# Performance work log

Measured on AMD Instinct MI355X. Metric: run time of the kernel, lower is better.

Reference implementation:

```python
import jax, jax.numpy as jnp
import numpy as np

D_MODEL, D_K, D_V = 1024, 64, 64
B, S = 2, 4096
NEG = 1e9


def setup_inputs() -> dict:
    key = jax.random.key(0)
    ks = jax.random.split(key, 10)
    Q = jax.random.normal(ks[0], (B, S, D_MODEL), dtype=jnp.float32)
    K = jax.random.normal(ks[1], (B, S, D_MODEL), dtype=jnp.float32)
    V = jax.random.normal(ks[2], (B, S, D_MODEL), dtype=jnp.float32)
    mask = jax.random.randint(ks[3], (B, S, S), 0, 2, dtype=jnp.int32)
    sc = 1.0 / np.sqrt(D_MODEL)
    Wq = jax.random.normal(ks[4], (D_K, D_MODEL), dtype=jnp.float32) * sc
    bq = jnp.zeros((D_K,), dtype=jnp.float32)
    Wk = jax.random.normal(ks[5], (D_K, D_MODEL), dtype=jnp.float32) * sc
    bk = jnp.zeros((D_K,), dtype=jnp.float32)
    Wv = jax.random.normal(ks[6], (D_V, D_MODEL), dtype=jnp.float32) * sc
    bv = jnp.zeros((D_V,), dtype=jnp.float32)
    return {"Q": Q, "K": K, "V": V, "mask": mask,
            "Wq": Wq, "bq": bq, "Wk": Wk, "bk": bk, "Wv": Wv, "bv": bv}


def reference(Q, K, V, mask, Wq, bq, Wk, bk, Wv, bv):
    # Linear projections: q,k -> [B,S,d_k], v -> [B,S,d_v]
    q = jnp.einsum('bsm,km->bsk', Q, Wq) + bq
    k = jnp.einsum('bsm,km->bsk', K, Wk) + bk
    v = jnp.einsum('bsm,vm->bsv', V, Wv) + bv
    # Scaled dot-product scores [B,S,S]
    x = jnp.einsum('bqk,bsk->bqs', q, k) / jnp.sqrt(jnp.float32(D_K))
    m = mask.astype(x.dtype)
    x = x * m - NEG * (1.0 - m)
    x = jax.nn.softmax(x, axis=2)
    y = jnp.einsum('bqs,bsv->bqv', x, v)
    return y
```

## Files before the change

### kernel.cpp

```cpp
#include <hip/hip_runtime.h>

typedef unsigned short u16;
typedef unsigned long long u64;
typedef __bf16 bf16x8 __attribute__((ext_vector_type(8)));
typedef float f32x4 __attribute__((ext_vector_type(4)));
typedef int i32x4 __attribute__((ext_vector_type(4)));

#define MFMA16(a, b, c) __builtin_amdgcn_mfma_f32_16x16x32_bf16((a), (b), (c), 0, 0, 0)

__device__ __forceinline__ bf16x8 ld8(const u16* p) {
    return *reinterpret_cast<const bf16x8*>(p);
}

__device__ __forceinline__ unsigned pk2(float a, float b) {
    unsigned short ua = __builtin_bit_cast(unsigned short, (__bf16)a);
    unsigned short ub = __builtin_bit_cast(unsigned short, (__bf16)b);
    return (unsigned)ua | ((unsigned)ub << 16);
}

__device__ __forceinline__ bf16x8 cvt8(f32x4 a, f32x4 b) {
    bf16x8 r;
    r[0] = (__bf16)a[0]; r[1] = (__bf16)a[1]; r[2] = (__bf16)a[2]; r[3] = (__bf16)a[3];
    r[4] = (__bf16)b[0]; r[5] = (__bf16)b[1]; r[6] = (__bf16)b[2]; r[7] = (__bf16)b[3];
    return r;
}

__device__ __forceinline__ f32x4 ntf4(const float* p) {
    return __builtin_nontemporal_load(reinterpret_cast<const f32x4*>(p));
}
__device__ __forceinline__ i32x4 nti4(const int* p) {
    return __builtin_nontemporal_load(reinterpret_cast<const i32x4*>(p));
}

__global__ __launch_bounds__(256) void wcvt_kernel(
    const float* __restrict__ Wq, const float* __restrict__ Wk,
    const float* __restrict__ Wv, u16* __restrict__ wb)
{
    const int t = blockIdx.x * 256 + threadIdx.x;
    const int mat = t >> 13;
    const int idx = (t & 8191) * 8;
    const float* src = (mat == 0) ? Wq : (mat == 1) ? Wk : Wv;
    const f32x4 a = *(const f32x4*)(src + idx);
    const f32x4 b = *(const f32x4*)(src + idx + 4);
    uint4 o;
    o.x = pk2(a[0], a[1]); o.y = pk2(a[2], a[3]);
    o.z = pk2(b[0], b[1]); o.w = pk2(b[2], b[3]);
    *reinterpret_cast<uint4*>(wb + (size_t)mat * 65536 + idx) = o;
}

__global__ __launch_bounds__(256) void fused_kernel(
    const float* __restrict__ Q, const float* __restrict__ K, const float* __restrict__ V,
    const float* __restrict__ bq, const float* __restrict__ bk, const float* __restrict__ bv,
    const u16* __restrict__ wb, const int* __restrict__ mask,
    u16* __restrict__ qb, u16* __restrict__ kb, u16* __restrict__ vtb,
    u64* __restrict__ bits)
{
    const int lane = threadIdx.x & 63, w = threadIdx.x >> 6;

    if (blockIdx.x >= 384) {
        const int row = (blockIdx.x - 384) * 4 + w;
        const int* mp = mask + (size_t)row * 4096 + lane * 4;
        u64* op = bits + (size_t)row * 64;

        i32x4 h0[8], h1[8];
        #pragma unroll
        for (int j = 0; j < 8; ++j) h0[j] = nti4(mp + j * 256);
        #pragma unroll
        for (int j = 0; j < 8; ++j) h1[j] = nti4(mp + 2048 + j * 256);

        u64 mine0 = 0, mine1 = 0;
        #pragma unroll
        for (int j = 0; j < 8; ++j) {
            const u64 b0 = __ballot(h0[j][0] != 0);
            const u64 b1 = __ballot(h0[j][1] != 0);
            const u64 b2 = __ballot(h0[j][2] != 0);
            const u64 b3 = __ballot(h0[j][3] != 0);
            if (lane == j * 4 + 0) mine0 = b0;
            if (lane == j * 4 + 1) mine0 = b1;
            if (lane == j * 4 + 2) mine0 = b2;
            if (lane == j * 4 + 3) mine0 = b3;
            const u64 c0 = __ballot(h1[j][0] != 0);
            const u64 c1 = __ballot(h1[j][1] != 0);
            const u64 c2 = __ballot(h1[j][2] != 0);
            const u64 c3 = __ballot(h1[j][3] != 0);
            if (lane == j * 4 + 0) mine1 = c0;
            if (lane == j * 4 + 1) mine1 = c1;
            if (lane == j * 4 + 2) mine1 = c2;
            if (lane == j * 4 + 3) mine1 = c3;
        }
        if (lane < 32) { op[lane] = mine0; op[32 + lane] = mine1; }
        return;
    }

    const int mat  = blockIdx.x >> 7;
    const int tile = blockIdx.x & 127;
    const int c = lane & 15, g = lane >> 4;

    const float* X = (mat == 0) ? Q : (mat == 1) ? K : V;
    const u16*   W = wb + (size_t)mat * 65536;

    const int rw = tile * 64 + w * 16;
    const float* xp = X + (size_t)(rw + c) * 1024 + g * 8;
    const u16*   wp = W + (size_t)c * 1024 + g * 8;

    f32x4 acc[4] = {};

    f32x4 A[4], B[4];
    #pragma unroll
    for (int j = 0; j < 4; ++j) {
        A[j] = ntf4(xp + j * 32);
        B[j] = ntf4(xp + j * 32 + 4);
    }

    #pragma unroll
    for (int kk = 0; kk < 32; ++kk) {
        const bf16x8 a = cvt8(A[kk & 3], B[kk & 3]);
        if (kk < 28) {
            A[kk & 3] = ntf4(xp + (kk + 4) * 32);
            B[kk & 3] = ntf4(xp + (kk + 4) * 32 + 4);
        }
        const u16* wk = wp + kk * 32;
        if (mat < 2) {
            #pragma unroll
            for (int t = 0; t < 4; ++t)
                acc[t] = MFMA16(a, ld8(wk + t * 16384), acc[t]);
        } else {
            #pragma unroll
            for (int t = 0; t < 4; ++t)
                acc[t] = MFMA16(ld8(wk + t * 16384), a, acc[t]);
        }
    }

    if (mat < 2) {
        const float* bias = (mat == 0) ? bq : bk;
        u16* dst = (mat == 0) ? qb : kb;
        #pragma unroll
        for (int t = 0; t < 4; ++t) {
            const float bz = bias[t * 16 + c];
            #pragma unroll
            for (int r = 0; r < 4; ++r) {
                const int row = rw + g * 4 + r;
                dst[(size_t)row * 64 + t * 16 + c] =
                    __builtin_bit_cast(u16, (__bf16)(acc[t][r] + bz));
            }
        }
    } else {
        const int sg = rw + c;
        const int bidx = sg >> 12, sin = sg & 4095;
        #pragma unroll
        for (int t = 0; t < 4; ++t) {
            #pragma unroll
            for (int r = 0; r < 4; ++r) {
                const int dv = t * 16 + g * 4 + r;
                vtb[(size_t)(bidx * 64 + dv) * 4096 + sin] =
                    __builtin_bit_cast(u16, (__bf16)(acc[t][r] + bv[dv]));
            }
        }
    }
}

__global__ __launch_bounds__(256) void attn_kernel(
    const u64* __restrict__ bits, const u16* __restrict__ qb,
    const u16* __restrict__ kb, const u16* __restrict__ vtb,
    float* __restrict__ pacc, float* __restrict__ pm, float* __restrict__ pl)
{
    __shared__ uint2 plds[4][128];
    const int lane = threadIdx.x & 63, w = threadIdx.x >> 6;
    const int c = lane & 15, g = lane >> 4;
    const int gw    = blockIdx.x * 4 + w;
    const int strip = gw >> 3;
    const int chunk = gw & 7;
    const int b     = strip >> 8;
    const int q0    = (strip & 255) * 16;
    const int sBase = chunk * 512;
    const float SSC = 0.18033688011112042f;

    const u16* qrow = qb + (size_t)((b << 12) + q0 + c) * 64 + g * 8;
    const bf16x8 qf0 = ld8(qrow);
    const bf16x8 qf1 = ld8(qrow + 32);

    const u16* kfp = kb  + (((size_t)b << 12) + sBase + c) * 64 + g * 8;
    const u16* vfp = vtb + (size_t)(b * 64 + c) * 4096 + sBase + g * 8;

    const u64* bp = bits + (size_t)((b << 12) + q0 + c) * 64 + chunk * 8;
    const u64 Wd0 = bp[0], Wd1 = bp[1], Wd2 = bp[2], Wd3 = bp[3];
    const u64 Wd4 = bp[4], Wd5 = bp[5], Wd6 = bp[6], Wd7 = bp[7];

    f32x4 acc0 = {}, acc1 = {}, acc2 = {}, acc3 = {};
    const f32x4 zf = {};
    float m_run = -__builtin_inff(), l_run = 0.f;

    bf16x8 k00 = ld8(kfp),            k01 = ld8(kfp + 32);
    bf16x8 k10 = ld8(kfp + 16 * 64),  k11 = ld8(kfp + 16 * 64 + 32);

    #pragma unroll
    for (int half = 0; half < 2; ++half) {
        const u64 Wr0 = half ? Wd4 : Wd0;
        const u64 Wr1 = half ? Wd5 : Wd1;
        const u64 Wr2 = half ? Wd6 : Wd2;
        const u64 Wr3 = half ? Wd7 : Wd3;
        #pragma unroll 1
        for (int it2 = 0; it2 < 8; ++it2) {
            const int it = half * 8 + it2;

            const u16* vp = vfp + it * 32;
            const bf16x8 v0 = ld8(vp);
            const bf16x8 v1 = ld8(vp + 16 * 4096);
            const bf16x8 v2 = ld8(vp + 32 * 4096);
            const bf16x8 v3 = ld8(vp + 48 * 4096);

            f32x4 d0 = MFMA16(k00, qf0, zf);
            d0 = MFMA16(k01, qf1, d0);
            f32x4 d1 = MFMA16(k10, qf0, zf);
            d1 = MFMA16(k11, qf1, d1);

            const int no = (it < 15) ? (it + 1) * 2048 : it * 2048;
            k00 = ld8(kfp + no);            k01 = ld8(kfp + no + 32);
            k10 = ld8(kfp + no + 16 * 64);  k11 = ld8(kfp + no + 16 * 64 + 32);

            const int sh = it2 * 8 + g;
            const unsigned t0 = (unsigned)(Wr0 >> sh);
            const unsigned t1 = (unsigned)(Wr1 >> sh);
            const unsigned t2 = (unsigned)(Wr2 >> sh);
            const unsigned t3 = (unsigned)(Wr3 >> sh);

            const float x0 = (t0 & 1u)  ? d0[0] * SSC : -1e9f;
            const float x1 = (t1 & 1u)  ? d0[1] * SSC : -1e9f;
            const float x2 = (t2 & 1u)  ? d0[2] * SSC : -1e9f;
            const float x3 = (t3 & 1u)  ? d0[3] * SSC : -1e9f;
            const float x4 = (t0 & 16u) ? d1[0] * SSC : -1e9f;
            const float x5 = (t1 & 16u) ? d1[1] * SSC : -1e9f;
            const float x6 = (t2 & 16u) ? d1[2] * SSC : -1e9f;
            const float x7 = (t3 & 16u) ? d1[3] * SSC : -1e9f;

            float tm = fmaxf(fmaxf(fmaxf(x0, x1), fmaxf(x2, x3)),
                             fmaxf(fmaxf(x4, x5), fmaxf(x6, x7)));
            tm = fmaxf(tm, __shfl_xor(tm, 16));
            tm = fmaxf(tm, __shfl_xor(tm, 32));
            const float m_new = fmaxf(m_run, tm);
            const float f = exp2f(m_run - m_new);

            const float p0 = exp2f(x0 - m_new), p1 = exp2f(x1 - m_new);
            const float p2 = exp2f(x2 - m_new), p3 = exp2f(x3 - m_new);
            const float p4 = exp2f(x4 - m_new), p5 = exp2f(x5 - m_new);
            const float p6 = exp2f(x6 - m_new), p7 = exp2f(x7 - m_new);
            float rs = ((p0 + p1) + (p2 + p3)) + ((p4 + p5) + (p6 + p7));
            rs += __shfl_xor(rs, 16);
            rs += __shfl_xor(rs, 32);
            l_run = l_run * f + rs;
            m_run = m_new;

            plds[w][c * 8 + ( g      ^ (c & 7))] = make_uint2(pk2(p0, p1), pk2(p2, p3));
            plds[w][c * 8 + ((g + 4) ^ (c & 7))] = make_uint2(pk2(p4, p5), pk2(p6, p7));

            if (__any(f < 1.0f)) {
                const float f0 = __shfl(f, g * 4 + 0);
                const float f1 = __shfl(f, g * 4 + 1);
                const float f2 = __shfl(f, g * 4 + 2);
                const float f3 = __shfl(f, g * 4 + 3);
                acc0[0] *= f0; acc0[1] *= f1; acc0[2] *= f2; acc0[3] *= f3;
                acc1[0] *= f0; acc1[1] *= f1; acc1[2] *= f2; acc1[3] *= f3;
                acc2[0] *= f0; acc2[1] *= f1; acc2[2] *= f2; acc2[3] *= f3;
                acc3[0] *= f0; acc3[1] *= f1; acc3[2] *= f2; acc3[3] *= f3;
            }

            union { uint2 u[2]; bf16x8 v; } pa;
            pa.u[0] = plds[w][c * 8 + ((2 * g    ) ^ (c & 7))];
            pa.u[1] = plds[w][c * 8 + ((2 * g + 1) ^ (c & 7))];

            acc0 = MFMA16(pa.v, v0, acc0);
            acc1 = MFMA16(pa.v, v1, acc1);
            acc2 = MFMA16(pa.v, v2, acc2);
            acc3 = MFMA16(pa.v, v3, acc3);
        }
    }

    const size_t pidx = (size_t)(strip * 8 + chunk) * 16;
    #pragma unroll
    for (int r = 0; r < 4; ++r) {
        const size_t row = pidx + g * 4 + r;
        pacc[row * 64 +  0 + c] = acc0[r];
        pacc[row * 64 + 16 + c] = acc1[r];
        pacc[row * 64 + 32 + c] = acc2[r];
        pacc[row * 64 + 48 + c] = acc3[r];
    }
    if (lane < 16) {
        pm[pidx + c] = m_run;
        pl[pidx + c] = l_run;
    }
}

__global__ __launch_bounds__(256) void comb_kernel(
    const float* __restrict__ pacc, const float* __restrict__ pm,
    const float* __restrict__ pl, float* __restrict__ out)
{
    const int t = blockIdx.x * 256 + threadIdx.x;
    const int r = t >> 6, dv = t & 63;
    const int strip = r >> 4, qi = r & 15;
    const int base = strip * 128 + qi;
    float mv[8];
    float M = -__builtin_inff();
    #pragma unroll
    for (int cc = 0; cc < 8; ++cc) { mv[cc] = pm[base + cc * 16]; M = fmaxf(M, mv[cc]); }
    float num = 0.f, den = 0.f;
    #pragma unroll
    for (int cc = 0; cc < 8; ++cc) {
        const float wgt = exp2f(mv[cc] - M);
        num += wgt * pacc[(size_t)(base + cc * 16) * 64 + dv];
        den += wgt * pl[base + cc * 16];
    }
    out[t] = num / den;
}

extern "C" void kernel_launch(void* const* d_in, const int* in_sizes, int n_in,
                              void* d_out, int out_size, void* d_ws, size_t ws_size,
                              hipStream_t stream)
{
    const float* Q    = (const float*)d_in[0];
    const float* K    = (const float*)d_in[1];
    const float* V    = (const float*)d_in[2];
    const int*   mask = (const int*)d_in[3];
    const float* Wq   = (const float*)d_in[4];
    const float* bq   = (const float*)d_in[5];
    const float* Wk   = (const float*)d_in[6];
    const float* bk   = (const float*)d_in[7];
    const float* Wv   = (const float*)d_in[8];
    const float* bv   = (const float*)d_in[9];
    float* out = (float*)d_out;

    char* ws = (char*)d_ws;
    u16*   wb   = (u16*)(ws);
    u16*   qb   = (u16*)(ws + 393216);
    u16*   kb   = (u16*)(ws + 393216 + 1048576);
    u16*   vtb  = (u16*)(ws + 393216 + 2097152);
    u64*   bits = (u64*)(ws + 4194304);
    float* pm   = (float*)(ws + 8388608);
    float* pl   = (float*)(ws + 8388608 + 262144);
    float* pacc = (float*)(ws + 8388608 + 524288);

    wcvt_kernel<<<96, 256, 0, stream>>>(Wq, Wk, Wv, wb);
    fused_kernel<<<2432, 256, 0, stream>>>(Q, K, V, bq, bk, bv, wb, mask,
                                           qb, kb, vtb, bits);
    attn_kernel<<<1024, 256, 0, stream>>>(bits, qb, kb, vtb, pacc, pm, pl);
    comb_kernel<<<2048, 256, 0, stream>>>(pacc, pm, pl, out);
}
```

Baseline: 141.5 us.

## Split projection K-dimension in two and add a reduction kernel; shrink mask-packing waves

The projection GEMM now splits the 1024-wide reduction across two blocks per tile, doubling the projection blocks from 384 to 768. Partial sums go to an fp32 workspace, and a new reduction kernel adds bias and writes the bf16 q/k/v^T outputs. Mask packing now gives each wave a quarter row with fewer live registers, which raises block count and occupancy. The cost is an extra kernel launch and about 12 MB of extra partial-sum traffic.

```diff
diff --git a/kernel.cpp b/kernel.cpp
--- a/kernel.cpp
+++ b/kernel.cpp
@@ -50,61 +50,48 @@
 
 __global__ __launch_bounds__(256) void fused_kernel(
     const float* __restrict__ Q, const float* __restrict__ K, const float* __restrict__ V,
-    const float* __restrict__ bq, const float* __restrict__ bk, const float* __restrict__ bv,
     const u16* __restrict__ wb, const int* __restrict__ mask,
-    u16* __restrict__ qb, u16* __restrict__ kb, u16* __restrict__ vtb,
-    u64* __restrict__ bits)
+    float* __restrict__ pws, u64* __restrict__ bits)
 {
     const int lane = threadIdx.x & 63, w = threadIdx.x >> 6;
 
-    if (blockIdx.x >= 384) {
-        const int row = (blockIdx.x - 384) * 4 + w;
-        const int* mp = mask + (size_t)row * 4096 + lane * 4;
-        u64* op = bits + (size_t)row * 64;
-
-        i32x4 h0[8], h1[8];
+    if (blockIdx.x >= 768) {
+        const int gw = (blockIdx.x - 768) * 4 + w;
+        const int* mp = mask + (size_t)gw * 1024 + lane * 4;
+        u64* op = bits + (size_t)gw * 16;
+
+        i32x4 cur = nti4(mp);
         #pragma unroll
-        for (int j = 0; j < 8; ++j) h0[j] = nti4(mp + j * 256);
-        #pragma unroll
-        for (int j = 0; j < 8; ++j) h1[j] = nti4(mp + 2048 + j * 256);
-
-        u64 mine0 = 0, mine1 = 0;
-        #pragma unroll
-        for (int j = 0; j < 8; ++j) {
-            const u64 b0 = __ballot(h0[j][0] != 0);
-            const u64 b1 = __ballot(h0[j][1] != 0);
-            const u64 b2 = __ballot(h0[j][2] != 0);
-            const u64 b3 = __ballot(h0[j][3] != 0);
-            if (lane == j * 4 + 0) mine0 = b0;
-            if (lane == j * 4 + 1) mine0 = b1;
-            if (lane == j * 4 + 2) mine0 = b2;
-            if (lane == j * 4 + 3) mine0 = b3;
-            const u64 c0 = __ballot(h1[j][0] != 0);
-            const u64 c1 = __ballot(h1[j][1] != 0);
-            const u64 c2 = __ballot(h1[j][2] != 0);
-            const u64 c3 = __ballot(h1[j][3] != 0);
-            if (lane == j * 4 + 0) mine1 = c0;
-            if (lane == j * 4 + 1) mine1 = c1;
-            if (lane == j * 4 + 2) mine1 = c2;
-            if (lane == j * 4 + 3) mine1 = c3;
+        for (int i = 0; i < 4; ++i) {
+            const i32x4 m4 = cur;
+            if (i < 3) cur = nti4(mp + (i + 1) * 256);
+            const u64 b0 = __ballot(m4[0] != 0);
+            const u64 b1 = __ballot(m4[1] != 0);
+            const u64 b2 = __ballot(m4[2] != 0);
+            const u64 b3 = __ballot(m4[3] != 0);
+            u64 myb = b0;
+            if (lane == 1) myb = b1;
+            if (lane == 2) myb = b2;
+            if (lane == 3) myb = b3;
+            if (lane < 4) op[i * 4 + lane] = myb;
         }
-        if (lane < 32) { op[lane] = mine0; op[32 + lane] = mine1; }
         return;
     }
 
-    const int mat  = blockIdx.x >> 7;
-    const int tile = blockIdx.x & 127;
+    const int mat  = blockIdx.x / 256;
+    const int rem  = blockIdx.x & 255;
+    const int tile = rem >> 1;
+    const int ks   = rem & 1;
     const int c = lane & 15, g = lane >> 4;
 
     const float* X = (mat == 0) ? Q : (mat == 1) ? K : V;
     const u16*   W = wb + (size_t)mat * 65536;
 
     const int rw = tile * 64 + w * 16;
-    const float* xp = X + (size_t)(rw + c) * 1024 + g * 8;
-    const u16*   wp = W + (size_t)c * 1024 + g * 8;
+    const float* xp = X + (size_t)(rw + c) * 1024 + ks * 512 + g * 8;
+    const u16*   wp = W + (size_t)c * 1024 + ks * 512 + g * 8;
 
     f32x4 acc[4] = {};
-
     f32x4 A[4], B[4];
     #pragma unroll
     for (int j = 0; j < 4; ++j) {
@@ -113,9 +100,9 @@
     }
 
     #pragma unroll
-    for (int kk = 0; kk < 32; ++kk) {
+    for (int kk = 0; kk < 16; ++kk) {
         const bf16x8 a = cvt8(A[kk & 3], B[kk & 3]);
-        if (kk < 28) {
+        if (kk < 12) {
             A[kk & 3] = ntf4(xp + (kk + 4) * 32);
             B[kk & 3] = ntf4(xp + (kk + 4) * 32 + 4);
         }
@@ -131,31 +118,43 @@
         }
     }
 
+    const size_t wave = (size_t)((mat * 128 + tile) * 4 + w);
+    float* pp = pws + wave * 2048 + ks;
+    #pragma unroll
+    for (int t = 0; t < 4; ++t) {
+        #pragma unroll
+        for (int r = 0; r < 4; ++r)
+            pp[(t * 256 + (g * 4 + r) * 16 + c) * 2] = acc[t][r];
+    }
+}
+
+__global__ __launch_bounds__(256) void projred_kernel(
+    const float* __restrict__ pws,
+    const float* __restrict__ bq, const float* __restrict__ bk, const float* __restrict__ bv,
+    u16* __restrict__ qb, u16* __restrict__ kb, u16* __restrict__ vtb)
+{
+    const int tid = blockIdx.x * 256 + threadIdx.x;
+    const int wave = tid >> 10;
+    const int idx  = tid & 1023;
+    const int t = idx >> 8, row16 = (idx >> 4) & 15, c = idx & 15;
+    const int mat  = wave >> 9;
+    const int tile = (wave >> 2) & 127;
+    const int w    = wave & 3;
+    const int rw   = tile * 64 + w * 16;
+
+    const float sum = pws[tid * 2] + pws[tid * 2 + 1];
+
     if (mat < 2) {
         const float* bias = (mat == 0) ? bq : bk;
         u16* dst = (mat == 0) ? qb : kb;
-        #pragma unroll
-        for (int t = 0; t < 4; ++t) {
-            const float bz = bias[t * 16 + c];
-            #pragma unroll
-            for (int r = 0; r < 4; ++r) {
-                const int row = rw + g * 4 + r;
-                dst[(size_t)row * 64 + t * 16 + c] =
-                    __builtin_bit_cast(u16, (__bf16)(acc[t][r] + bz));
-            }
-        }
+        const int row = rw + row16;
+        dst[(size_t)row * 64 + t * 16 + c] =
+            __builtin_bit_cast(u16, (__bf16)(sum + bias[t * 16 + c]));
     } else {
+        const int dv = t * 16 + row16;
         const int sg = rw + c;
-        const int bidx = sg >> 12, sin = sg & 4095;
-        #pragma unroll
-        for (int t = 0; t < 4; ++t) {
-            #pragma unroll
-            for (int r = 0; r < 4; ++r) {
-                const int dv = t * 16 + g * 4 + r;
-                vtb[(size_t)(bidx * 64 + dv) * 4096 + sin] =
-                    __builtin_bit_cast(u16, (__bf16)(acc[t][r] + bv[dv]));
-            }
-        }
+        vtb[(size_t)((sg >> 12) * 64 + dv) * 4096 + (sg & 4095)] =
+            __builtin_bit_cast(u16, (__bf16)(sum + bv[dv]));
     }
 }
 
@@ -337,10 +336,11 @@
     float* pm   = (float*)(ws + 8388608);
     float* pl   = (float*)(ws + 8388608 + 262144);
     float* pacc = (float*)(ws + 8388608 + 524288);
+    float* pws  = (float*)(ws + 8388608 + 524288 + 16777216);
 
     wcvt_kernel<<<96, 256, 0, stream>>>(Wq, Wk, Wv, wb);
-    fused_kernel<<<2432, 256, 0, stream>>>(Q, K, V, bq, bk, bv, wb, mask,
-                                           qb, kb, vtb, bits);
+    fused_kernel<<<8960, 256, 0, stream>>>(Q, K, V, wb, mask, pws, bits);
+    projred_kernel<<<6144, 256, 0, stream>>>(pws, bq, bk, bv, qb, kb, vtb);
     attn_kernel<<<1024, 256, 0, stream>>>(bits, qb, kb, vtb, pacc, pm, pl);
     comb_kernel<<<2048, 256, 0, stream>>>(pacc, pm, pl, out);
 }
```

New measurement: 151.1 us. +6.8%, slower.

## Stage projection input rows in swizzled LDS and split output columns across waves

Applied to the files above, without the earlier changes.

The projection part of the fused kernel used to have each wave own 16 rows and all 64 output columns, streaming the fp32 input directly into registers. Each block now loads a 16-row tile of X with fully coalesced loads, converts it to bf16, and stores it in XOR-swizzled shared memory. Each of the four waves then computes one 16-column slice of the output from that shared tile. This raises the projection block count fourfold and adds a block barrier and an LDS round trip, in exchange for better coalescing and more parallelism. Each wave now issues a quarter of the MFMAs, so per-wave arithmetic intensity is lower.

```diff
diff --git a/kernel.cpp b/kernel.cpp
--- a/kernel.cpp
+++ b/kernel.cpp
@@ -16,13 +16,6 @@
     unsigned short ua = __builtin_bit_cast(unsigned short, (__bf16)a);
     unsigned short ub = __builtin_bit_cast(unsigned short, (__bf16)b);
     return (unsigned)ua | ((unsigned)ub << 16);
-}
-
-__device__ __forceinline__ bf16x8 cvt8(f32x4 a, f32x4 b) {
-    bf16x8 r;
-    r[0] = (__bf16)a[0]; r[1] = (__bf16)a[1]; r[2] = (__bf16)a[2]; r[3] = (__bf16)a[3];
-    r[4] = (__bf16)b[0]; r[5] = (__bf16)b[1]; r[6] = (__bf16)b[2]; r[7] = (__bf16)b[3];
-    return r;
 }
 
 __device__ __forceinline__ f32x4 ntf4(const float* p) {
@@ -55,10 +48,11 @@
     u16* __restrict__ qb, u16* __restrict__ kb, u16* __restrict__ vtb,
     u64* __restrict__ bits)
 {
+    __shared__ uint2 xlds[16][256];
     const int lane = threadIdx.x & 63, w = threadIdx.x >> 6;
 
-    if (blockIdx.x >= 384) {
-        const int row = (blockIdx.x - 384) * 4 + w;
+    if (blockIdx.x >= 1536) {
+        const int row = (blockIdx.x - 1536) * 4 + w;
         const int* mp = mask + (size_t)row * 4096 + lane * 4;
         u64* op = bits + (size_t)row * 64;
 
@@ -92,69 +86,53 @@
         return;
     }
 
-    const int mat  = blockIdx.x >> 7;
-    const int tile = blockIdx.x & 127;
+    const int mat  = blockIdx.x >> 9;
+    const int tile = blockIdx.x & 511;
+    const int r0   = tile * 16;
+    const int t    = threadIdx.x;
+    const float* X = (mat == 0) ? Q : (mat == 1) ? K : V;
+
+    f32x4 st[16];
+    const float* xp = X + (size_t)r0 * 1024 + t * 4;
+    #pragma unroll
+    for (int i = 0; i < 16; ++i) st[i] = ntf4(xp + i * 1024);
+
+    #pragma unroll
+    for (int i = 0; i < 16; ++i) {
+        xlds[i][(((t >> 1) ^ (i & 7)) << 1) | (t & 1)] =
+            make_uint2(pk2(st[i][0], st[i][1]), pk2(st[i][2], st[i][3]));
+    }
+    __syncthreads();
+
     const int c = lane & 15, g = lane >> 4;
-
-    const float* X = (mat == 0) ? Q : (mat == 1) ? K : V;
-    const u16*   W = wb + (size_t)mat * 65536;
-
-    const int rw = tile * 64 + w * 16;
-    const float* xp = X + (size_t)(rw + c) * 1024 + g * 8;
-    const u16*   wp = W + (size_t)c * 1024 + g * 8;
-
-    f32x4 acc[4] = {};
-
-    f32x4 A[4], B[4];
-    #pragma unroll
-    for (int j = 0; j < 4; ++j) {
-        A[j] = ntf4(xp + j * 32);
-        B[j] = ntf4(xp + j * 32 + 4);
-    }
-
+    const u16* wp = wb + (size_t)mat * 65536 + (size_t)(w * 16 + c) * 1024 + g * 8;
+
+    f32x4 acc = {};
     #pragma unroll
     for (int kk = 0; kk < 32; ++kk) {
-        const bf16x8 a = cvt8(A[kk & 3], B[kk & 3]);
-        if (kk < 28) {
-            A[kk & 3] = ntf4(xp + (kk + 4) * 32);
-            B[kk & 3] = ntf4(xp + (kk + 4) * 32 + 4);
-        }
-        const u16* wk = wp + kk * 32;
-        if (mat < 2) {
-            #pragma unroll
-            for (int t = 0; t < 4; ++t)
-                acc[t] = MFMA16(a, ld8(wk + t * 16384), acc[t]);
-        } else {
-            #pragma unroll
-            for (int t = 0; t < 4; ++t)
-                acc[t] = MFMA16(ld8(wk + t * 16384), a, acc[t]);
-        }
+        const bf16x8 a = ld8((const u16*)&xlds[c][((kk * 4 + g) ^ (c & 7)) << 1]);
+        const bf16x8 wf = ld8(wp + kk * 32);
+        if (mat < 2) acc = MFMA16(a, wf, acc);
+        else         acc = MFMA16(wf, a, acc);
     }
 
     if (mat < 2) {
         const float* bias = (mat == 0) ? bq : bk;
         u16* dst = (mat == 0) ? qb : kb;
-        #pragma unroll
-        for (int t = 0; t < 4; ++t) {
-            const float bz = bias[t * 16 + c];
-            #pragma unroll
-            for (int r = 0; r < 4; ++r) {
-                const int row = rw + g * 4 + r;
-                dst[(size_t)row * 64 + t * 16 + c] =
-                    __builtin_bit_cast(u16, (__bf16)(acc[t][r] + bz));
-            }
+        const float bz = bias[w * 16 + c];
+        #pragma unroll
+        for (int r = 0; r < 4; ++r) {
+            dst[(size_t)(r0 + g * 4 + r) * 64 + w * 16 + c] =
+                __builtin_bit_cast(u16, (__bf16)(acc[r] + bz));
         }
     } else {
-        const int sg = rw + c;
+        const int sg = r0 + c;
         const int bidx = sg >> 12, sin = sg & 4095;
         #pragma unroll
-        for (int t = 0; t < 4; ++t) {
-            #pragma unroll
-            for (int r = 0; r < 4; ++r) {
-                const int dv = t * 16 + g * 4 + r;
-                vtb[(size_t)(bidx * 64 + dv) * 4096 + sin] =
-                    __builtin_bit_cast(u16, (__bf16)(acc[t][r] + bv[dv]));
-            }
+        for (int r = 0; r < 4; ++r) {
+            const int dv = w * 16 + g * 4 + r;
+            vtb[(size_t)(bidx * 64 + dv) * 4096 + sin] =
+                __builtin_bit_cast(u16, (__bf16)(acc[r] + bv[dv]));
         }
     }
 }
@@ -339,7 +317,7 @@
     float* pacc = (float*)(ws + 8388608 + 524288);
 
     wcvt_kernel<<<96, 256, 0, stream>>>(Wq, Wk, Wv, wb);
-    fused_kernel<<<2432, 256, 0, stream>>>(Q, K, V, bq, bk, bv, wb, mask,
+    fused_kernel<<<3584, 256, 0, stream>>>(Q, K, V, bq, bk, bv, wb, mask,
                                            qb, kb, vtb, bits);
     attn_kernel<<<1024, 256, 0, stream>>>(bits, qb, kb, vtb, pacc, pm, pl);
     comb_kernel<<<2048, 256, 0, stream>>>(pacc, pm, pl, out);
```

After: 133.8 us. -5.4%, faster.
